# Performance work log

Hardware: AMD Instinct MI355X
Metric: run time of the kernel (lower is better)

## Reference

```python
import jax, jax.numpy as jnp
import numpy as np

N, F_IN, F_OUT = 8192, 512, 256


def setup_inputs() -> dict:
    key = jax.random.key(0)
    k1, k2, k3, k4 = jax.random.split(key, 4)
    x = jax.random.normal(k1, (N, F_IN), dtype=jnp.float32)
    adj = jax.random.randint(k2, (N, N), 0, 2, dtype=jnp.int32)
    # xavier_uniform with gain=1.414
    limW = 1.414 * np.sqrt(6.0 / (F_IN + F_OUT))
    W = jax.random.uniform(k3, (F_IN, F_OUT), dtype=jnp.float32, minval=-limW, maxval=limW)
    lima = 1.414 * np.sqrt(6.0 / (2 * F_OUT + 1))
    a = jax.random.uniform(k4, (2 * F_OUT, 1), dtype=jnp.float32, minval=-lima, maxval=lima)
    return {"x": x, "adj": adj, "W": W, "a": a}


def reference(x, adj, W, a):
    # h = x @ W : [N, F_out]
    h = x @ W
    f_out = h.shape[1]
    # additive score a^T [h_i ; h_j] is separable: (h @ a_l)_i + (h @ a_r)_j
    f_src = h @ a[:f_out, 0]   # [N]
    f_dst = h @ a[f_out:, 0]   # [N]
    e = jax.nn.leaky_relu(f_src[:, None] + f_dst[None, :], negative_slope=0.2)  # [N, N]
    e = jnp.where(adj > 0, e, jnp.float32(-9e15))
    attention = jax.nn.softmax(e, axis=1)  # row-wise over neighbors
    # dropout(p=0.6) is identity in eval mode
    h_prime = attention @ h  # [N, F_out]
    return h_prime
```

## Files before the change

### kernel.cpp

```cpp
#include <hip/hip_runtime.h>
#include <hip/hip_bf16.h>

#define NN 8192
#define FIN 512
#define FOUT 256

typedef __attribute__((ext_vector_type(8))) short short8;
typedef __attribute__((ext_vector_type(4))) float float4v;
typedef __attribute__((ext_vector_type(16))) float float16v;

__device__ __forceinline__ short f2bf(float f) {
    union { float f; unsigned u; } v; v.f = f;
    unsigned r = (v.u + 0x7FFFu + ((v.u >> 16) & 1u)) >> 16;
    return (short)r;
}

__global__ __launch_bounds__(256) void wt_kernel(const float* __restrict__ W,
                                                 short* __restrict__ Wt) {
    __shared__ short tile[32][33];
    int tx = threadIdx.x & 31, ty = threadIdx.x >> 5;
    int k0 = blockIdx.x * 32, n0 = blockIdx.y * 32;
#pragma unroll
    for (int r = 0; r < 32; r += 8)
        tile[ty + r][tx] = f2bf(W[(size_t)(k0 + ty + r) * FOUT + n0 + tx]);
    __syncthreads();
#pragma unroll
    for (int r = 0; r < 32; r += 8)
        Wt[(size_t)(n0 + ty + r) * FIN + k0 + tx] = tile[tx][ty + r];
}

__global__ __launch_bounds__(256) void h_kernel(const float* __restrict__ x,
                                                const short* __restrict__ Wt,
                                                const float* __restrict__ a,
                                                short* __restrict__ h_t,
                                                float* __restrict__ f_src,
                                                float* __restrict__ f_dst) {
    int wave = (blockIdx.x << 2) + (threadIdx.x >> 6);
    int lane = threadIdx.x & 63;
    int m0 = (wave & 511) << 4;
    int n0 = (wave >> 9) << 6;
    int lr = lane & 15, lq = lane >> 4;

    const float* xrow = x + (size_t)(m0 + lr) * FIN + lq * 8;
    const short* wbase = Wt + (size_t)(n0 + lr) * FIN + lq * 8;

    float4v acc[4] = {};
    for (int k0 = 0; k0 < FIN; k0 += 32) {
        float4v xa = *(const float4v*)(xrow + k0);
        float4v xb = *(const float4v*)(xrow + k0 + 4);
        short8 av;
        av[0] = f2bf(xa[0]); av[1] = f2bf(xa[1]); av[2] = f2bf(xa[2]); av[3] = f2bf(xa[3]);
        av[4] = f2bf(xb[0]); av[5] = f2bf(xb[1]); av[6] = f2bf(xb[2]); av[7] = f2bf(xb[3]);
#pragma unroll
        for (int ct = 0; ct < 4; ct++) {
            short8 bv = *(const short8*)(wbase + (size_t)ct * 16 * FIN + k0);
            acc[ct] = __builtin_amdgcn_mfma_f32_16x16x32_bf16(av, bv, acc[ct], 0, 0, 0);
        }
    }
    float s_part[4] = {0.f, 0.f, 0.f, 0.f};
    float d_part[4] = {0.f, 0.f, 0.f, 0.f};
#pragma unroll
    for (int ct = 0; ct < 4; ct++) {
        int n = n0 + ct * 16 + lr;
        float al = a[n], ar = a[FOUT + n];
#pragma unroll
        for (int reg = 0; reg < 4; reg++) {
            float hv = acc[ct][reg];
            s_part[reg] = fmaf(hv, al, s_part[reg]);
            d_part[reg] = fmaf(hv, ar, d_part[reg]);
            h_t[(size_t)n * NN + (m0 + lq * 4 + reg)] = f2bf(hv);
        }
    }
#pragma unroll
    for (int off = 1; off < 16; off <<= 1) {
#pragma unroll
        for (int reg = 0; reg < 4; reg++) {
            s_part[reg] += __shfl_xor(s_part[reg], off);
            d_part[reg] += __shfl_xor(d_part[reg], off);
        }
    }
    const float LOG2E = 1.4426950408889634f;
    if (lr == 0) {
#pragma unroll
        for (int reg = 0; reg < 4; reg++) {
            atomicAdd(&f_src[m0 + lq * 4 + reg], s_part[reg] * LOG2E);
            atomicAdd(&f_dst[m0 + lq * 4 + reg], d_part[reg] * LOG2E);
        }
    }
}

__global__ __launch_bounds__(256, 2) void gat_kernel(const int* __restrict__ adj,
                                                     const short* __restrict__ h_t,
                                                     const float* __restrict__ f_src,
                                                     const float* __restrict__ f_dst,
                                                     float* __restrict__ Opart,
                                                     float* __restrict__ lpart,
                                                     int jlen) {
    __shared__ short Bb[2][256 * 64];

    const int t = threadIdx.x;
    const int lane = t & 63;
    const int w = t >> 6;
    const int l31 = lane & 31, lq = lane >> 5;
    const int i0 = blockIdx.x * 128;
    const int slice = blockIdx.y;
    const int jbase = slice * jlen;
    const int myrow = i0 + w * 32 + l31;
    const int rsw = l31 & 7;
    const int swz = t & 7;
    const int nchunk = jlen >> 6;

    const float fs = f_src[myrow];
    const int* adjL = adj + (size_t)myrow * NN + jbase + lq * 8;
    const float* fdL = f_dst + jbase + lq * 8;
    const short* hrow = h_t + (size_t)t * NN + jbase;

    float16v acc[8] = {};
    float lp = 0.f;

    int4 aj[2][2];
    float4 fd[2][2];
    aj[0][0] = *(const int4*)(adjL);       aj[0][1] = *(const int4*)(adjL + 4);
    fd[0][0] = *(const float4*)(fdL);      fd[0][1] = *(const float4*)(fdL + 4);
    aj[1][0] = *(const int4*)(adjL + 16);  aj[1][1] = *(const int4*)(adjL + 20);
    fd[1][0] = *(const float4*)(fdL + 16); fd[1][1] = *(const float4*)(fdL + 20);

    {
#pragma unroll
        for (int q = 0; q < 8; q++) {
            short8 b = *(const short8*)(hrow + q * 8);
            *(short8*)(&Bb[0][0] + t * 64 + ((q ^ swz) << 3)) = b;
        }
    }
    __syncthreads();

    for (int c = 0; c < nchunk; ++c) {
        short* curb = &Bb[c & 1][0];
        short* nxtb = &Bb[(c & 1) ^ 1][0];
        const int jn = (c + 1 < nchunk) ? (c + 1) * 64 : 0;

        auto kstep = [&](int kk) {
            const int s = kk & 1;
            const int4 A0 = aj[s][0], A1 = aj[s][1];
            const float4 F0 = fd[s][0], F1 = fd[s][1];
            int off = (c * 4 + kk + 2) * 16;
            if (off >= jlen) off -= jlen;
            aj[s][0] = *(const int4*)(adjL + off);
            aj[s][1] = *(const int4*)(adjL + off + 4);
            fd[s][0] = *(const float4*)(fdL + off);
            fd[s][1] = *(const float4*)(fdL + off + 4);

            const int* ai0 = (const int*)&A0;
            const int* ai1 = (const int*)&A1;
            const float* ff0 = (const float*)&F0;
            const float* ff1 = (const float*)&F1;
            short8 af;
#pragma unroll
            for (int q = 0; q < 4; q++) {
                float y = fs + ff0[q];
                y = fmaxf(y, 0.2f * y);
                float e = exp2f(y);
                float p = ai0[q] ? e : 0.f;
                lp += p;
                af[q] = f2bf(p);
            }
#pragma unroll
            for (int q = 0; q < 4; q++) {
                float y = fs + ff1[q];
                y = fmaxf(y, 0.2f * y);
                float e = exp2f(y);
                float p = ai1[q] ? e : 0.f;
                lp += p;
                af[4 + q] = f2bf(p);
            }
            const int cb = ((kk * 2 + lq) ^ rsw) << 3;
#pragma unroll
            for (int nt = 0; nt < 8; nt++) {
                short8 b = *(const short8*)(curb + (nt * 32 + l31) * 64 + cb);
                acc[nt] = __builtin_amdgcn_mfma_f32_32x32x16_bf16(af, b, acc[nt], 0, 0, 0);
            }
        };

        short8 s0 = *(const short8*)(hrow + jn + 0);
        short8 s1 = *(const short8*)(hrow + jn + 8);
        short8 s2 = *(const short8*)(hrow + jn + 16);
        short8 s3 = *(const short8*)(hrow + jn + 24);
        kstep(0);
        kstep(1);
        *(short8*)(nxtb + t * 64 + ((0 ^ swz) << 3)) = s0;
        *(short8*)(nxtb + t * 64 + ((1 ^ swz) << 3)) = s1;
        *(short8*)(nxtb + t * 64 + ((2 ^ swz) << 3)) = s2;
        *(short8*)(nxtb + t * 64 + ((3 ^ swz) << 3)) = s3;
        short8 s4 = *(const short8*)(hrow + jn + 32);
        short8 s5 = *(const short8*)(hrow + jn + 40);
        short8 s6 = *(const short8*)(hrow + jn + 48);
        short8 s7 = *(const short8*)(hrow + jn + 56);
        kstep(2);
        kstep(3);
        *(short8*)(nxtb + t * 64 + ((4 ^ swz) << 3)) = s4;
        *(short8*)(nxtb + t * 64 + ((5 ^ swz) << 3)) = s5;
        *(short8*)(nxtb + t * 64 + ((6 ^ swz) << 3)) = s6;
        *(short8*)(nxtb + t * 64 + ((7 ^ swz) << 3)) = s7;

        asm volatile("s_waitcnt lgkmcnt(0)" ::: "memory");
        asm volatile("s_barrier" ::: "memory");
    }

    lp += __shfl_xor(lp, 32);
    if (lq == 0) lpart[(size_t)slice * NN + myrow] = lp;

    float* ob = Opart + ((size_t)slice * NN + i0 + w * 32) * FOUT;
#pragma unroll
    for (int nt = 0; nt < 8; nt++) {
        int n = nt * 32 + l31;
#pragma unroll
        for (int reg = 0; reg < 16; reg++) {
            int row = (reg & 3) + 8 * (reg >> 2) + 4 * lq;
            ob[(size_t)row * FOUT + n] = acc[nt][reg];
        }
    }
}

__global__ __launch_bounds__(256) void combine_kernel(const float* __restrict__ Opart,
                                                      const float* __restrict__ lpart,
                                                      float* __restrict__ out, int slices) {
    int i = blockIdx.x, n = threadIdx.x;
    float o = 0.f, l = 0.f;
    for (int s = 0; s < slices; s++) {
        o += Opart[((size_t)s * NN + i) * FOUT + n];
        l += lpart[(size_t)s * NN + i];
    }
    out[(size_t)i * FOUT + n] = o / l;
}

extern "C" void kernel_launch(void* const* d_in, const int* in_sizes, int n_in,
                              void* d_out, int out_size, void* d_ws, size_t ws_size,
                              hipStream_t stream) {
    const float* x   = (const float*)d_in[0];
    const int*   adj = (const int*)d_in[1];
    const float* W   = (const float*)d_in[2];
    const float* a   = (const float*)d_in[3];
    float* out = (float*)d_out;

    char* ws = (char*)d_ws;
    short* h_t   = (short*)ws;
    short* Wt    = (short*)(ws + (4u << 20));
    float* f_src = (float*)(ws + (4u << 20) + (256u << 10));
    float* f_dst = (float*)(ws + (4u << 20) + (288u << 10));
    float* lpart = (float*)(ws + (4u << 20) + (320u << 10));
    float* Opart = (float*)(ws + (8u << 20));

    const size_t OSLICE = (size_t)NN * FOUT * 4;
    int slices = 2;
    if (ws_size >= (8u << 20) + 8 * OSLICE) slices = 8;
    else if (ws_size >= (8u << 20) + 4 * OSLICE) slices = 4;
    int jlen = NN / slices;

    hipMemsetAsync(f_src, 0, 2 * NN * sizeof(float), stream);
    wt_kernel<<<dim3(FIN / 32, FOUT / 32), 256, 0, stream>>>(W, Wt);
    h_kernel<<<512, 256, 0, stream>>>(x, Wt, a, h_t, f_src, f_dst);
    gat_kernel<<<dim3(NN / 128, slices), 256, 0, stream>>>(adj, h_t, f_src, f_dst,
                                                           Opart, lpart, jlen);
    combine_kernel<<<NN, 256, 0, stream>>>(Opart, lpart, out, slices);
}
```

Before: 474.7 us.

## Pack adjacency to bitmask, drop LDS staging in GAT kernel, split waves over features

```diff
diff --git a/kernel.cpp b/kernel.cpp
--- a/kernel.cpp
+++ b/kernel.cpp
@@ -13,6 +13,18 @@
     union { float f; unsigned u; } v; v.f = f;
     unsigned r = (v.u + 0x7FFFu + ((v.u >> 16) & 1u)) >> 16;
     return (short)r;
+}
+
+__global__ __launch_bounds__(256) void pack_kernel(const int* __restrict__ adj,
+                                                   unsigned long long* __restrict__ pk64) {
+    const int tid = blockIdx.x * 256 + threadIdx.x;
+    const int stride = 2048 * 256;
+#pragma unroll 4
+    for (int k = 0; k < (NN * NN) / stride; ++k) {
+        int idx = tid + k * stride;
+        unsigned long long m = __ballot(adj[idx] != 0);
+        if ((threadIdx.x & 63) == 0) pk64[idx >> 6] = m;
+    }
 }
 
 __global__ __launch_bounds__(256) void wt_kernel(const float* __restrict__ W,
@@ -38,13 +50,13 @@
     int wave = (blockIdx.x << 2) + (threadIdx.x >> 6);
     int lane = threadIdx.x & 63;
     int m0 = (wave & 511) << 4;
-    int n0 = (wave >> 9) << 6;
+    int n0 = (wave >> 9) << 5;
     int lr = lane & 15, lq = lane >> 4;
 
     const float* xrow = x + (size_t)(m0 + lr) * FIN + lq * 8;
     const short* wbase = Wt + (size_t)(n0 + lr) * FIN + lq * 8;
 
-    float4v acc[4] = {};
+    float4v acc[2] = {};
     for (int k0 = 0; k0 < FIN; k0 += 32) {
         float4v xa = *(const float4v*)(xrow + k0);
         float4v xb = *(const float4v*)(xrow + k0 + 4);
@@ -52,7 +64,7 @@
         av[0] = f2bf(xa[0]); av[1] = f2bf(xa[1]); av[2] = f2bf(xa[2]); av[3] = f2bf(xa[3]);
         av[4] = f2bf(xb[0]); av[5] = f2bf(xb[1]); av[6] = f2bf(xb[2]); av[7] = f2bf(xb[3]);
 #pragma unroll
-        for (int ct = 0; ct < 4; ct++) {
+        for (int ct = 0; ct < 2; ct++) {
             short8 bv = *(const short8*)(wbase + (size_t)ct * 16 * FIN + k0);
             acc[ct] = __builtin_amdgcn_mfma_f32_16x16x32_bf16(av, bv, acc[ct], 0, 0, 0);
         }
@@ -60,7 +72,7 @@
     float s_part[4] = {0.f, 0.f, 0.f, 0.f};
     float d_part[4] = {0.f, 0.f, 0.f, 0.f};
 #pragma unroll
-    for (int ct = 0; ct < 4; ct++) {
+    for (int ct = 0; ct < 2; ct++) {
         int n = n0 + ct * 16 + lr;
         float al = a[n], ar = a[FOUT + n];
 #pragma unroll
@@ -89,129 +101,73 @@
     }
 }
 
-__global__ __launch_bounds__(256, 2) void gat_kernel(const int* __restrict__ adj,
+__global__ __launch_bounds__(512, 4) void gat_kernel(const unsigned long long* __restrict__ pk64,
                                                      const short* __restrict__ h_t,
                                                      const float* __restrict__ f_src,
                                                      const float* __restrict__ f_dst,
                                                      float* __restrict__ Opart,
                                                      float* __restrict__ lpart,
                                                      int jlen) {
-    __shared__ short Bb[2][256 * 64];
-
     const int t = threadIdx.x;
     const int lane = t & 63;
     const int w = t >> 6;
     const int l31 = lane & 31, lq = lane >> 5;
+    const int wr = w & 3, wc = w >> 2;
     const int i0 = blockIdx.x * 128;
     const int slice = blockIdx.y;
     const int jbase = slice * jlen;
-    const int myrow = i0 + w * 32 + l31;
-    const int rsw = l31 & 7;
-    const int swz = t & 7;
+    const int r = i0 + wr * 32 + l31;
     const int nchunk = jlen >> 6;
 
-    const float fs = f_src[myrow];
-    const int* adjL = adj + (size_t)myrow * NN + jbase + lq * 8;
+    const float fs = f_src[r];
+    const unsigned long long* pkRow = pk64 + (size_t)r * (NN / 64) + (jbase >> 6);
+    const short* hb = h_t + (size_t)(wc * 128 + l31) * NN + jbase + lq * 8;
     const float* fdL = f_dst + jbase + lq * 8;
-    const short* hrow = h_t + (size_t)t * NN + jbase;
-
-    float16v acc[8] = {};
+
+    float16v acc[4] = {};
     float lp = 0.f;
 
-    int4 aj[2][2];
-    float4 fd[2][2];
-    aj[0][0] = *(const int4*)(adjL);       aj[0][1] = *(const int4*)(adjL + 4);
-    fd[0][0] = *(const float4*)(fdL);      fd[0][1] = *(const float4*)(fdL + 4);
-    aj[1][0] = *(const int4*)(adjL + 16);  aj[1][1] = *(const int4*)(adjL + 20);
-    fd[1][0] = *(const float4*)(fdL + 16); fd[1][1] = *(const float4*)(fdL + 20);
-
-    {
-#pragma unroll
-        for (int q = 0; q < 8; q++) {
-            short8 b = *(const short8*)(hrow + q * 8);
-            *(short8*)(&Bb[0][0] + t * 64 + ((q ^ swz) << 3)) = b;
-        }
-    }
-    __syncthreads();
-
     for (int c = 0; c < nchunk; ++c) {
-        short* curb = &Bb[c & 1][0];
-        short* nxtb = &Bb[(c & 1) ^ 1][0];
-        const int jn = (c + 1 < nchunk) ? (c + 1) * 64 : 0;
-
-        auto kstep = [&](int kk) {
-            const int s = kk & 1;
-            const int4 A0 = aj[s][0], A1 = aj[s][1];
-            const float4 F0 = fd[s][0], F1 = fd[s][1];
-            int off = (c * 4 + kk + 2) * 16;
-            if (off >= jlen) off -= jlen;
-            aj[s][0] = *(const int4*)(adjL + off);
-            aj[s][1] = *(const int4*)(adjL + off + 4);
-            fd[s][0] = *(const float4*)(fdL + off);
-            fd[s][1] = *(const float4*)(fdL + off + 4);
-
-            const int* ai0 = (const int*)&A0;
-            const int* ai1 = (const int*)&A1;
-            const float* ff0 = (const float*)&F0;
-            const float* ff1 = (const float*)&F1;
+        unsigned long long bm = pkRow[c];
+        unsigned bmlo = (unsigned)bm, bmhi = (unsigned)(bm >> 32);
+#pragma unroll
+        for (int kk = 0; kk < 4; ++kk) {
+            const int jo = c * 64 + kk * 16;
+            float4 f0 = *(const float4*)(fdL + jo);
+            float4 f1 = *(const float4*)(fdL + jo + 4);
+            unsigned w32 = (kk < 2) ? bmlo : bmhi;
+            unsigned m8 = (w32 >> ((kk & 1) * 16 + lq * 8)) & 0xffu;
+
             short8 af;
-#pragma unroll
-            for (int q = 0; q < 4; q++) {
-                float y = fs + ff0[q];
+            const float* ff0 = (const float*)&f0;
+            const float* ff1 = (const float*)&f1;
+#pragma unroll
+            for (int q = 0; q < 8; ++q) {
+                float fdv = (q < 4) ? ff0[q] : ff1[q - 4];
+                float y = fs + fdv;
                 y = fmaxf(y, 0.2f * y);
                 float e = exp2f(y);
-                float p = ai0[q] ? e : 0.f;
+                float p = (m8 & (1u << q)) ? e : 0.f;
                 lp += p;
                 af[q] = f2bf(p);
             }
-#pragma unroll
-            for (int q = 0; q < 4; q++) {
-                float y = fs + ff1[q];
-                y = fmaxf(y, 0.2f * y);
-                float e = exp2f(y);
-                float p = ai1[q] ? e : 0.f;
-                lp += p;
-                af[4 + q] = f2bf(p);
-            }
-            const int cb = ((kk * 2 + lq) ^ rsw) << 3;
-#pragma unroll
-            for (int nt = 0; nt < 8; nt++) {
-                short8 b = *(const short8*)(curb + (nt * 32 + l31) * 64 + cb);
-                acc[nt] = __builtin_amdgcn_mfma_f32_32x32x16_bf16(af, b, acc[nt], 0, 0, 0);
-            }
-        };
-
-        short8 s0 = *(const short8*)(hrow + jn + 0);
-        short8 s1 = *(const short8*)(hrow + jn + 8);
-        short8 s2 = *(const short8*)(hrow + jn + 16);
-        short8 s3 = *(const short8*)(hrow + jn + 24);
-        kstep(0);
-        kstep(1);
-        *(short8*)(nxtb + t * 64 + ((0 ^ swz) << 3)) = s0;
-        *(short8*)(nxtb + t * 64 + ((1 ^ swz) << 3)) = s1;
-        *(short8*)(nxtb + t * 64 + ((2 ^ swz) << 3)) = s2;
-        *(short8*)(nxtb + t * 64 + ((3 ^ swz) << 3)) = s3;
-        short8 s4 = *(const short8*)(hrow + jn + 32);
-        short8 s5 = *(const short8*)(hrow + jn + 40);
-        short8 s6 = *(const short8*)(hrow + jn + 48);
-        short8 s7 = *(const short8*)(hrow + jn + 56);
-        kstep(2);
-        kstep(3);
-        *(short8*)(nxtb + t * 64 + ((4 ^ swz) << 3)) = s4;
-        *(short8*)(nxtb + t * 64 + ((5 ^ swz) << 3)) = s5;
-        *(short8*)(nxtb + t * 64 + ((6 ^ swz) << 3)) = s6;
-        *(short8*)(nxtb + t * 64 + ((7 ^ swz) << 3)) = s7;
-
-        asm volatile("s_waitcnt lgkmcnt(0)" ::: "memory");
-        asm volatile("s_barrier" ::: "memory");
+            short8 b0 = *(const short8*)(hb + 0 * 32 * NN + jo);
+            short8 b1 = *(const short8*)(hb + 1 * 32 * NN + jo);
+            short8 b2 = *(const short8*)(hb + 2 * 32 * NN + jo);
+            short8 b3 = *(const short8*)(hb + 3 * 32 * NN + jo);
+            acc[0] = __builtin_amdgcn_mfma_f32_32x32x16_bf16(af, b0, acc[0], 0, 0, 0);
+            acc[1] = __builtin_amdgcn_mfma_f32_32x32x16_bf16(af, b1, acc[1], 0, 0, 0);
+            acc[2] = __builtin_amdgcn_mfma_f32_32x32x16_bf16(af, b2, acc[2], 0, 0, 0);
+            acc[3] = __builtin_amdgcn_mfma_f32_32x32x16_bf16(af, b3, acc[3], 0, 0, 0);
+        }
     }
 
     lp += __shfl_xor(lp, 32);
-    if (lq == 0) lpart[(size_t)slice * NN + myrow] = lp;
-
-    float* ob = Opart + ((size_t)slice * NN + i0 + w * 32) * FOUT;
-#pragma unroll
-    for (int nt = 0; nt < 8; nt++) {
+    if (wc == 0 && lq == 0) lpart[(size_t)slice * NN + r] = lp;
+
+    float* ob = Opart + ((size_t)slice * NN + i0 + wr * 32) * FOUT + wc * 128;
+#pragma unroll
+    for (int nt = 0; nt < 4; nt++) {
         int n = nt * 32 + l31;
 #pragma unroll
         for (int reg = 0; reg < 16; reg++) {
@@ -248,18 +204,17 @@
     float* f_src = (float*)(ws + (4u << 20) + (256u << 10));
     float* f_dst = (float*)(ws + (4u << 20) + (288u << 10));
     float* lpart = (float*)(ws + (4u << 20) + (320u << 10));
-    float* Opart = (float*)(ws + (8u << 20));
-
-    const size_t OSLICE = (size_t)NN * FOUT * 4;
-    int slices = 2;
-    if (ws_size >= (8u << 20) + 8 * OSLICE) slices = 8;
-    else if (ws_size >= (8u << 20) + 4 * OSLICE) slices = 4;
-    int jlen = NN / slices;
+    unsigned long long* pk64 = (unsigned long long*)(ws + (6u << 20));
+    float* Opart = (float*)(ws + (16u << 20));
+
+    const int slices = 4;
+    const int jlen = NN / slices;
 
     hipMemsetAsync(f_src, 0, 2 * NN * sizeof(float), stream);
+    pack_kernel<<<2048, 256, 0, stream>>>(adj, pk64);
     wt_kernel<<<dim3(FIN / 32, FOUT / 32), 256, 0, stream>>>(W, Wt);
-    h_kernel<<<512, 256, 0, stream>>>(x, Wt, a, h_t, f_src, f_dst);
-    gat_kernel<<<dim3(NN / 128, slices), 256, 0, stream>>>(adj, h_t, f_src, f_dst,
+    h_kernel<<<1024, 256, 0, stream>>>(x, Wt, a, h_t, f_src, f_dst);
+    gat_kernel<<<dim3(NN / 128, slices), 512, 0, stream>>>(pk64, h_t, f_src, f_dst,
                                                            Opart, lpart, jlen);
     combine_kernel<<<NN, 256, 0, stream>>>(Opart, lpart, out, slices);
 }
```

Result: slower. 570.7 us (+20.2%).
